# Performance work log

Measured on AMD Instinct MI355X. Metric: run time of the kernel, lower is better.

The kernel has to match this reference:

```python
import jax, jax.numpy as jnp
import numpy as np

N_NODES = 100000
N_EDGES = 1600000
D = 128          # in = hidden = out channels
N_LAYERS = 3


def setup_inputs() -> dict:
    key = jax.random.key(0)
    ks = jax.random.split(key, 20)
    inp = {
        "x": jax.random.normal(ks[0], (N_NODES, D), jnp.float32),
        "edge_index": jax.random.randint(ks[1], (2, N_EDGES), 0, N_NODES, dtype=jnp.int64),
    }
    s = 1.0 / np.sqrt(D)
    k = 2
    for l in range(N_LAYERS):
        inp[f"w1_{l}"] = jax.random.normal(ks[k], (D, D), jnp.float32) * s; k += 1
        inp[f"b1_{l}"] = jnp.zeros((D,), jnp.float32)
        inp[f"w2_{l}"] = jax.random.normal(ks[k], (D, D), jnp.float32) * s; k += 1
        inp[f"b2_{l}"] = jnp.zeros((D,), jnp.float32)
    # JK concat: 3 layers * D channels -> out D
    inp["jk_w"] = jax.random.normal(ks[k], (N_LAYERS * D, D), jnp.float32) * (1.0 / np.sqrt(N_LAYERS * D))
    inp["jk_b"] = jnp.zeros((D,), jnp.float32)
    return inp


def _gin_layer(x, src, dst, w1, b1, w2, b2):
    # GINConv, eps=0: h = (1+eps)*x + sum_{j in N(i)} x_j ; then MLP Lin-ReLU-Lin
    agg = jax.ops.segment_sum(x[src], dst, num_segments=N_NODES)  # [N, D]
    h = x + agg
    h = jax.nn.relu(h @ w1 + b1)
    return h @ w2 + b2


def reference(x, edge_index, w1_0, b1_0, w2_0, b2_0, w1_1, b1_1, w2_1, b2_1,
              w1_2, b1_2, w2_2, b2_2, jk_w, jk_b):
    src, dst = edge_index[0], edge_index[1]
    layers = [(w1_0, b1_0, w2_0, b2_0), (w1_1, b1_1, w2_1, b2_1), (w1_2, b1_2, w2_2, b2_2)]
    xs = []
    for i, (w1, b1, w2, b2) in enumerate(layers):
        # dropout is identity in eval mode
        residual = x  # skip_proj is Identity since in==out channels
        x = _gin_layer(x, src, dst, w1, b1, w2, b2) + residual
        if i != N_LAYERS - 1:
            x = jax.nn.elu(x)
        xs.append(x)
    x = jnp.concatenate(xs, axis=-1)  # JK 'cat' -> [N, 3*D]
    return x @ jk_w + jk_b
```

## Files before the change

### kernel.cpp

```cpp
#include <hip/hip_runtime.h>

typedef __bf16 bf16x8 __attribute__((ext_vector_type(8)));
typedef float f32x4 __attribute__((ext_vector_type(4)));

#define CHUNK 4096
#define NBUCK 512

struct WPack { const float* p[9]; };

__device__ inline __bf16 f2bf(float f){ return (__bf16)f; }

__global__ __launch_bounds__(256) void conv_w_kernel(WPack pk, __bf16* __restrict__ wf){
  int tid = blockIdx.x*256 + threadIdx.x;
  int m = tid >> 14;
  int r = tid & 16383;
  int j = r & 7;
  int lane = (r >> 3) & 63;
  int ks = (r >> 9) & 3;
  int c = r >> 11;
  int k = ks*32 + ((lane>>4)<<3) + j;
  int col = (c<<4) + (lane & 15);
  wf[tid] = f2bf(pk.p[m][k*128 + col]);
}

__global__ __launch_bounds__(256) void f2b_kernel(const float* __restrict__ x, __bf16* __restrict__ xb, int n8){
  int i = blockIdx.x*256 + threadIdx.x;
  if (i >= n8) return;
  f32x4 a = ((const f32x4*)x)[2*i];
  f32x4 b = ((const f32x4*)x)[2*i+1];
  bf16x8 r;
  r[0]=f2bf(a[0]); r[1]=f2bf(a[1]); r[2]=f2bf(a[2]); r[3]=f2bf(a[3]);
  r[4]=f2bf(b[0]); r[5]=f2bf(b[1]); r[6]=f2bf(b[2]); r[7]=f2bf(b[3]);
  ((bf16x8*)xb)[i] = r;
}

__global__ __launch_bounds__(256) void p1_count(const int* __restrict__ ei, int E, int NBLK,
    int* __restrict__ cnt){
  __shared__ int h[NBUCK];
  int b = blockIdx.x, t = threadIdx.x;
  h[t] = 0; h[t + 256] = 0;
  __syncthreads();
  int base = b*CHUNK;
  int lim = E - base; if (lim > CHUNK) lim = CHUNK;
  for (int i = t; i < lim; i += 256)
    atomicAdd(&h[ei[E + base + i] >> 8], 1);
  __syncthreads();
  cnt[t*NBLK + b] = h[t];
  cnt[(t + 256)*NBLK + b] = h[t + 256];
}

__global__ __launch_bounds__(256) void scan1_kernel(const int* __restrict__ cnt, int* __restrict__ bsum, int L){
  __shared__ int sh[256];
  int b = blockIdx.x, t = threadIdx.x;
  int base = b*2048 + t*8;
  int s = 0;
  #pragma unroll
  for (int j = 0; j < 8; j++){ int i = base + j; if (i < L) s += cnt[i]; }
  sh[t] = s; __syncthreads();
  for (int off = 128; off > 0; off >>= 1){
    if (t < off) sh[t] += sh[t + off];
    __syncthreads();
  }
  if (t == 0) bsum[b] = sh[0];
}

__global__ __launch_bounds__(256) void scan2_kernel(const int* __restrict__ bsum, int* __restrict__ boff,
                                                    int NB, int* __restrict__ total_out){
  __shared__ int sh[256];
  int t = threadIdx.x;
  int v = (t < NB) ? bsum[t] : 0;
  sh[t] = v; __syncthreads();
  for (int off = 1; off < 256; off <<= 1){
    int u = (t >= off) ? sh[t - off] : 0;
    __syncthreads();
    sh[t] += u;
    __syncthreads();
  }
  if (t < NB) boff[t] = sh[t] - v;
  if (t == 255) *total_out = sh[255];
}

__global__ __launch_bounds__(256) void scan3_kernel(const int* __restrict__ cnt, const int* __restrict__ boff,
                                                    int* __restrict__ off, int L){
  __shared__ int sh[256];
  int b = blockIdx.x, t = threadIdx.x;
  int base = b*2048 + t*8;
  int loc[8]; int s = 0;
  #pragma unroll
  for (int j = 0; j < 8; j++){ int i = base + j; int d = (i < L) ? cnt[i] : 0; loc[j] = d; s += d; }
  sh[t] = s; __syncthreads();
  for (int o = 1; o < 256; o <<= 1){
    int u = (t >= o) ? sh[t - o] : 0;
    __syncthreads();
    sh[t] += u;
    __syncthreads();
  }
  int excl = boff[b] + sh[t] - s;
  #pragma unroll
  for (int j = 0; j < 8; j++){ int i = base + j; if (i < L) off[i] = excl; excl += loc[j]; }
}

__global__ __launch_bounds__(256) void p3_scatter(const int* __restrict__ ei, int E, int NBLK,
    const int* __restrict__ off, int* __restrict__ tpack){
  __shared__ int cur[NBUCK];
  int b = blockIdx.x, t = threadIdx.x;
  cur[t]       = off[t*NBLK + b];
  cur[t + 256] = off[(t + 256)*NBLK + b];
  __syncthreads();
  int base = b*CHUNK;
  int lim = E - base; if (lim > CHUNK) lim = CHUNK;
  for (int i = t; i < lim; i += 256){
    int s = ei[base + i];
    int d = ei[E + base + i];
    int p = atomicAdd(&cur[d >> 8], 1);
    tpack[p] = (s << 8) | (d & 255);
  }
}

__global__ __launch_bounds__(256) void p4_build(const int* __restrict__ tpack,
    const int* __restrict__ off, int NBLK, int E, int N,
    int* __restrict__ rs, int* __restrict__ csr){
  __shared__ int dc[256], sc[256];
  int q = blockIdx.x, t = threadIdx.x;
  int bstart = off[q*NBLK];
  int bend = (q == NBUCK-1) ? E : off[(q+1)*NBLK];
  dc[t] = 0;
  __syncthreads();
  for (int i = bstart + t; i < bend; i += 256)
    atomicAdd(&dc[tpack[i] & 255], 1);
  __syncthreads();
  int v = dc[t];
  sc[t] = v; __syncthreads();
  for (int o = 1; o < 256; o <<= 1){
    int u = (t >= o) ? sc[t - o] : 0;
    __syncthreads();
    sc[t] += u;
    __syncthreads();
  }
  int ex = sc[t] - v;
  int gd = q*256 + t;
  if (gd < N) rs[gd] = bstart + ex;
  __syncthreads();
  dc[t] = ex;
  __syncthreads();
  for (int i = bstart + t; i < bend; i += 256){
    int p = tpack[i];
    int r = atomicAdd(&dc[p & 255], 1);
    csr[bstart + r] = p >> 8;
  }
}

__global__ __launch_bounds__(256) void agg_kernel(const __bf16* __restrict__ xb,
    const int* __restrict__ rs, const int* __restrict__ csr,
    __bf16* __restrict__ hb, int N)
{
  int node = blockIdx.x*4 + (threadIdx.x >> 6);
  if (node >= N) return;
  int lane = threadIdx.x & 63;
  int quad = lane >> 4;
  int l16  = lane & 15;
  int s = rs[node], e = rs[node+1];
  float a[8] = {0.f,0.f,0.f,0.f,0.f,0.f,0.f,0.f};
  for (int base = s; base < e; base += 64){
    int idx = base + lane;
    int nb = (idx < e) ? csr[idx] : 0;
    int cnt = e - base; if (cnt > 64) cnt = 64;
    int t = 0;
    for (; t + 8 <= cnt; t += 8){
      int sA = __shfl(nb, t + quad);
      int sB = __shfl(nb, t + 4 + quad);
      bf16x8 vA = ((const bf16x8*)(xb + (long)sA*128))[l16];
      bf16x8 vB = ((const bf16x8*)(xb + (long)sB*128))[l16];
      #pragma unroll
      for (int j = 0; j < 8; j++) a[j] += (float)vA[j] + (float)vB[j];
    }
    for (; t < cnt; t += 4){
      int i = t + quad;
      int ic = (i < cnt) ? i : (cnt - 1);
      int sA = __shfl(nb, ic);
      bf16x8 vA = ((const bf16x8*)(xb + (long)sA*128))[l16];
      if (i < cnt){
        #pragma unroll
        for (int j = 0; j < 8; j++) a[j] += (float)vA[j];
      }
    }
  }
  if (quad == 0){
    bf16x8 sv = ((const bf16x8*)(xb + (long)node*128))[l16];
    #pragma unroll
    for (int j = 0; j < 8; j++) a[j] += (float)sv[j];
  }
  #pragma unroll
  for (int j = 0; j < 8; j++){
    a[j] += __shfl_xor(a[j], 16);
    a[j] += __shfl_xor(a[j], 32);
  }
  if (quad == 0){
    bf16x8 r;
    #pragma unroll
    for (int j = 0; j < 8; j++) r[j] = f2bf(a[j]);
    ((bf16x8*)(hb + (long)node*128))[l16] = r;
  }
}

template<int ACT2>
__global__ __launch_bounds__(256) void fused_mlp(const __bf16* __restrict__ A,
    const __bf16* __restrict__ wf1, const __bf16* __restrict__ wf2,
    const float* __restrict__ b1, const float* __restrict__ b2,
    const __bf16* __restrict__ res, __bf16* __restrict__ out, int M)
{
  __shared__ __bf16 H[128][136];
  int lane = threadIdx.x & 63;
  int wid = threadIdx.x >> 6;
  long row0 = (long)blockIdx.x * 128;
  const bf16x8* w1v = (const bf16x8*)wf1;
  const bf16x8* w2v = (const bf16x8*)wf2;
  bf16x8 bv1[2][4], bv2[2][4];
  #pragma unroll
  for (int c2 = 0; c2 < 2; c2++)
    #pragma unroll
    for (int ks = 0; ks < 4; ks++){
      bv1[c2][ks] = w1v[((wid*2 + c2)*4 + ks)*64 + lane];
      bv2[c2][ks] = w2v[((wid*2 + c2)*4 + ks)*64 + lane];
    }
  int col0 = wid*32 + (lane & 15);
  float bb1_0 = b1[col0], bb1_1 = b1[col0 + 16];
  float bb2_0 = b2[col0], bb2_1 = b2[col0 + 16];
  int koff = (lane >> 4) << 3;
  #pragma unroll 2
  for (int rt = 0; rt < 8; rt++){
    long row = row0 + rt*16 + (lane & 15);
    long rowc = (row < M) ? row : (long)(M-1);
    const __bf16* ap = A + rowc*128 + koff;
    bf16x8 av[4];
    #pragma unroll
    for (int ks = 0; ks < 4; ks++)
      av[ks] = *(const bf16x8*)(ap + ks*32);
    f32x4 acc0 = {0.f,0.f,0.f,0.f}, acc1 = {0.f,0.f,0.f,0.f};
    #pragma unroll
    for (int ks = 0; ks < 4; ks++){
      acc0 = __builtin_amdgcn_mfma_f32_16x16x32_bf16(av[ks], bv1[0][ks], acc0, 0, 0, 0);
      acc1 = __builtin_amdgcn_mfma_f32_16x16x32_bf16(av[ks], bv1[1][ks], acc1, 0, 0, 0);
    }
    int r0 = rt*16 + ((lane >> 4) << 2);
    #pragma unroll
    for (int c2 = 0; c2 < 2; c2++){
      f32x4 acc = c2 ? acc1 : acc0;
      int col = col0 + c2*16;
      float bb = c2 ? bb1_1 : bb1_0;
      #pragma unroll
      for (int i = 0; i < 4; i++)
        H[r0 + i][col] = f2bf(fmaxf(acc[i] + bb, 0.f));
    }
  }
  __syncthreads();
  #pragma unroll 2
  for (int rt = 0; rt < 8; rt++){
    int r = rt*16 + (lane & 15);
    bf16x8 av[4];
    #pragma unroll
    for (int ks = 0; ks < 4; ks++)
      av[ks] = *(const bf16x8*)(&H[r][ks*32 + koff]);
    f32x4 acc0 = {0.f,0.f,0.f,0.f}, acc1 = {0.f,0.f,0.f,0.f};
    #pragma unroll
    for (int ks = 0; ks < 4; ks++){
      acc0 = __builtin_amdgcn_mfma_f32_16x16x32_bf16(av[ks], bv2[0][ks], acc0, 0, 0, 0);
      acc1 = __builtin_amdgcn_mfma_f32_16x16x32_bf16(av[ks], bv2[1][ks], acc1, 0, 0, 0);
    }
    long orow0 = row0 + rt*16 + ((lane >> 4) << 2);
    #pragma unroll
    for (int c2 = 0; c2 < 2; c2++){
      f32x4 acc = c2 ? acc1 : acc0;
      int col = col0 + c2*16;
      float bb = c2 ? bb2_1 : bb2_0;
      #pragma unroll
      for (int i = 0; i < 4; i++){
        long orow = orow0 + i;
        if (orow < M){
          long idx = orow*128 + col;
          float v = acc[i] + bb + (float)res[idx];
          if (ACT2 == 2) v = (v > 0.f) ? v : (__expf(v) - 1.f);
          out[idx] = f2bf(v);
        }
      }
    }
  }
}

__global__ __launch_bounds__(256) void jk_gemm(const __bf16* __restrict__ y1,
    const __bf16* __restrict__ y2, const __bf16* __restrict__ y3,
    const __bf16* __restrict__ wf, const float* __restrict__ bias,
    float* __restrict__ out, int M)
{
  int lane = threadIdx.x & 63;
  int wid = threadIdx.x >> 6;
  long row0 = (long)blockIdx.x * 128;
  const bf16x8* wfv = (const bf16x8*)wf;
  bf16x8 bv[2][12];
  #pragma unroll
  for (int c2 = 0; c2 < 2; c2++)
    #pragma unroll
    for (int ks = 0; ks < 12; ks++)
      bv[c2][ks] = wfv[(size_t)(6 + (ks>>2))*2048 + (size_t)((wid*2 + c2)*4 + (ks&3))*64 + lane];
  int col0 = wid*32 + (lane & 15);
  float b0 = bias[col0], b1 = bias[col0 + 16];
  int koff = (lane >> 4) << 3;
  const __bf16* ys[3] = {y1, y2, y3};
  #pragma unroll 1
  for (int rt = 0; rt < 8; rt++){
    long row = row0 + rt*16 + (lane & 15);
    long rowc = (row < M) ? row : (long)(M-1);
    f32x4 acc0 = {0.f,0.f,0.f,0.f}, acc1 = {0.f,0.f,0.f,0.f};
    #pragma unroll
    for (int ks = 0; ks < 12; ks++){
      bf16x8 av = *(const bf16x8*)(ys[ks>>2] + rowc*128 + (ks&3)*32 + koff);
      acc0 = __builtin_amdgcn_mfma_f32_16x16x32_bf16(av, bv[0][ks], acc0, 0, 0, 0);
      acc1 = __builtin_amdgcn_mfma_f32_16x16x32_bf16(av, bv[1][ks], acc1, 0, 0, 0);
    }
    long orow0 = row0 + rt*16 + ((lane >> 4) << 2);
    #pragma unroll
    for (int c2 = 0; c2 < 2; c2++){
      f32x4 acc = c2 ? acc1 : acc0;
      int col = col0 + c2*16;
      float bb = c2 ? b1 : b0;
      #pragma unroll
      for (int i = 0; i < 4; i++){
        long orow = orow0 + i;
        if (orow < M)
          out[orow*128 + col] = acc[i] + bb;
      }
    }
  }
}

extern "C" void kernel_launch(void* const* d_in, const int* in_sizes, int n_in,
                              void* d_out, int out_size, void* d_ws, size_t ws_size,
                              hipStream_t stream)
{
  const float* x   = (const float*)d_in[0];
  const int*   ei  = (const int*)d_in[1];
  const float* w1[3] = {(const float*)d_in[2], (const float*)d_in[6], (const float*)d_in[10]};
  const float* b1[3] = {(const float*)d_in[3], (const float*)d_in[7], (const float*)d_in[11]};
  const float* w2[3] = {(const float*)d_in[4], (const float*)d_in[8], (const float*)d_in[12]};
  const float* b2[3] = {(const float*)d_in[5], (const float*)d_in[9], (const float*)d_in[13]};
  const float* jkw = (const float*)d_in[14];
  const float* jkb = (const float*)d_in[15];
  int N = in_sizes[0] / 128;
  int E = in_sizes[1] / 2;
  float* outp = (float*)d_out;

  char* wptr = (char*)d_ws;
  auto alloc = [&](size_t bytes)->void*{
    void* p = (void*)wptr; wptr += (bytes + 255) & ~(size_t)255; return p;
  };
  int NBLK = (E + CHUNK - 1) / CHUNK;
  int L = NBUCK * NBLK;
  int* rs    = (int*)alloc((size_t)(N+1)*4);
  int* csr   = (int*)alloc((size_t)E*4);
  int* tpack = (int*)alloc((size_t)E*4);
  int* cnt   = (int*)alloc((size_t)L*4);
  int* off   = (int*)alloc((size_t)L*4);
  __bf16* y[4];
  for (int i = 0; i < 4; i++) y[i] = (__bf16*)alloc((size_t)N*128*2);
  __bf16* hb = (__bf16*)alloc((size_t)N*128*2);
  __bf16* wf = (__bf16*)alloc((size_t)9*16384*2);
  int nsb = (L + 2047) / 2048;
  int* bsum = (int*)alloc((size_t)nsb*4);
  int* boff = (int*)alloc((size_t)nsb*4);

  WPack pk;
  pk.p[0] = w1[0]; pk.p[1] = w2[0];
  pk.p[2] = w1[1]; pk.p[3] = w2[1];
  pk.p[4] = w1[2]; pk.p[5] = w2[2];
  pk.p[6] = jkw; pk.p[7] = jkw + 16384; pk.p[8] = jkw + 32768;
  conv_w_kernel<<<576, 256, 0, stream>>>(pk, wf);

  f2b_kernel<<<(N*128/8 + 255)/256, 256, 0, stream>>>(x, y[0], N*128/8);

  p1_count<<<NBLK, 256, 0, stream>>>(ei, E, NBLK, cnt);
  scan1_kernel<<<nsb, 256, 0, stream>>>(cnt, bsum, L);
  scan2_kernel<<<1, 256, 0, stream>>>(bsum, boff, nsb, rs + N);
  scan3_kernel<<<nsb, 256, 0, stream>>>(cnt, boff, off, L);
  p3_scatter<<<NBLK, 256, 0, stream>>>(ei, E, NBLK, off, tpack);
  p4_build<<<NBUCK, 256, 0, stream>>>(tpack, off, NBLK, E, N, rs, csr);

  int gemm_blocks = (N + 127)/128;
  for (int l = 0; l < 3; l++){
    agg_kernel<<<(N + 3)/4, 256, 0, stream>>>(y[l], rs, csr, hb, N);
    if (l < 2)
      fused_mlp<2><<<gemm_blocks, 256, 0, stream>>>(hb, wf + (size_t)(2*l)*16384, wf + (size_t)(2*l+1)*16384,
                                                    b1[l], b2[l], y[l], y[l+1], N);
    else
      fused_mlp<0><<<gemm_blocks, 256, 0, stream>>>(hb, wf + (size_t)(2*l)*16384, wf + (size_t)(2*l+1)*16384,
                                                    b1[l], b2[l], y[l], y[l+1], N);
  }
  jk_gemm<<<gemm_blocks, 256, 0, stream>>>(y[1], y[2], y[3], wf, jkb, outp, N);
}
```

Before: 428.6 us.

## Fuse last GIN layer MLP with JK projection and merge prep kernels

The final layer's MLP now feeds the JK concat GEMM directly. Its output stays in shared memory, so the y3 buffer is never written to or re-read from global memory, and one launch is removed. The weight-conversion and input-conversion kernels are merged into a single launch, and the aggregation inner loop gets an unroll-2 pragma. In exchange the fused kernel uses about 68KB of LDS per block and holds more weight registers, which may lower occupancy.

```diff
diff --git a/kernel.cpp b/kernel.cpp
--- a/kernel.cpp
+++ b/kernel.cpp
@@ -10,28 +10,30 @@
 
 __device__ inline __bf16 f2bf(float f){ return (__bf16)f; }
 
-__global__ __launch_bounds__(256) void conv_w_kernel(WPack pk, __bf16* __restrict__ wf){
-  int tid = blockIdx.x*256 + threadIdx.x;
-  int m = tid >> 14;
-  int r = tid & 16383;
-  int j = r & 7;
-  int lane = (r >> 3) & 63;
-  int ks = (r >> 9) & 3;
-  int c = r >> 11;
-  int k = ks*32 + ((lane>>4)<<3) + j;
-  int col = (c<<4) + (lane & 15);
-  wf[tid] = f2bf(pk.p[m][k*128 + col]);
-}
-
-__global__ __launch_bounds__(256) void f2b_kernel(const float* __restrict__ x, __bf16* __restrict__ xb, int n8){
-  int i = blockIdx.x*256 + threadIdx.x;
-  if (i >= n8) return;
-  f32x4 a = ((const f32x4*)x)[2*i];
-  f32x4 b = ((const f32x4*)x)[2*i+1];
-  bf16x8 r;
-  r[0]=f2bf(a[0]); r[1]=f2bf(a[1]); r[2]=f2bf(a[2]); r[3]=f2bf(a[3]);
-  r[4]=f2bf(b[0]); r[5]=f2bf(b[1]); r[6]=f2bf(b[2]); r[7]=f2bf(b[3]);
-  ((bf16x8*)xb)[i] = r;
+__global__ __launch_bounds__(256) void prep_kernel(WPack pk, __bf16* __restrict__ wf,
+    const float* __restrict__ x, __bf16* __restrict__ xb, int n8){
+  int b = blockIdx.x, t = threadIdx.x;
+  if (b < 576){
+    int tid = b*256 + t;
+    int m = tid >> 14;
+    int r = tid & 16383;
+    int j = r & 7;
+    int lane = (r >> 3) & 63;
+    int ks = (r >> 9) & 3;
+    int c = r >> 11;
+    int k = ks*32 + ((lane>>4)<<3) + j;
+    int col = (c<<4) + (lane & 15);
+    wf[tid] = f2bf(pk.p[m][k*128 + col]);
+  } else {
+    int i = (b - 576)*256 + t;
+    if (i >= n8) return;
+    f32x4 a = ((const f32x4*)x)[2*i];
+    f32x4 bb = ((const f32x4*)x)[2*i+1];
+    bf16x8 r;
+    r[0]=f2bf(a[0]); r[1]=f2bf(a[1]); r[2]=f2bf(a[2]); r[3]=f2bf(a[3]);
+    r[4]=f2bf(bb[0]); r[5]=f2bf(bb[1]); r[6]=f2bf(bb[2]); r[7]=f2bf(bb[3]);
+    ((bf16x8*)xb)[i] = r;
+  }
 }
 
 __global__ __launch_bounds__(256) void p1_count(const int* __restrict__ ei, int E, int NBLK,
@@ -166,6 +168,7 @@
     int nb = (idx < e) ? csr[idx] : 0;
     int cnt = e - base; if (cnt > 64) cnt = 64;
     int t = 0;
+    #pragma unroll 2
     for (; t + 8 <= cnt; t += 8){
       int sA = __shfl(nb, t + quad);
       int sB = __shfl(nb, t + 4 + quad);
@@ -287,42 +290,117 @@
   }
 }
 
-__global__ __launch_bounds__(256) void jk_gemm(const __bf16* __restrict__ y1,
-    const __bf16* __restrict__ y2, const __bf16* __restrict__ y3,
-    const __bf16* __restrict__ wf, const float* __restrict__ bias,
-    float* __restrict__ out, int M)
+__global__ __launch_bounds__(256) void fused_mlp_jk(const __bf16* __restrict__ A,
+    const __bf16* __restrict__ y1g, const __bf16* __restrict__ y2g,
+    const __bf16* __restrict__ wf1, const __bf16* __restrict__ wf2,
+    const __bf16* __restrict__ wfjk,
+    const float* __restrict__ b1, const float* __restrict__ b2,
+    const float* __restrict__ jkb, float* __restrict__ out, int M)
 {
+  __shared__ __bf16 H[128][136];
+  __shared__ __bf16 Y3[128][136];
   int lane = threadIdx.x & 63;
   int wid = threadIdx.x >> 6;
   long row0 = (long)blockIdx.x * 128;
-  const bf16x8* wfv = (const bf16x8*)wf;
-  bf16x8 bv[2][12];
+  const bf16x8* w1v = (const bf16x8*)wf1;
+  const bf16x8* w2v = (const bf16x8*)wf2;
+  bf16x8 bv1[2][4], bv2[2][4];
   #pragma unroll
   for (int c2 = 0; c2 < 2; c2++)
     #pragma unroll
+    for (int ks = 0; ks < 4; ks++){
+      bv1[c2][ks] = w1v[((wid*2 + c2)*4 + ks)*64 + lane];
+      bv2[c2][ks] = w2v[((wid*2 + c2)*4 + ks)*64 + lane];
+    }
+  int col0 = wid*32 + (lane & 15);
+  float bb1_0 = b1[col0], bb1_1 = b1[col0 + 16];
+  float bb2_0 = b2[col0], bb2_1 = b2[col0 + 16];
+  int koff = (lane >> 4) << 3;
+  #pragma unroll 2
+  for (int rt = 0; rt < 8; rt++){
+    long row = row0 + rt*16 + (lane & 15);
+    long rowc = (row < M) ? row : (long)(M-1);
+    const __bf16* ap = A + rowc*128 + koff;
+    bf16x8 av[4];
+    #pragma unroll
+    for (int ks = 0; ks < 4; ks++)
+      av[ks] = *(const bf16x8*)(ap + ks*32);
+    f32x4 acc0 = {0.f,0.f,0.f,0.f}, acc1 = {0.f,0.f,0.f,0.f};
+    #pragma unroll
+    for (int ks = 0; ks < 4; ks++){
+      acc0 = __builtin_amdgcn_mfma_f32_16x16x32_bf16(av[ks], bv1[0][ks], acc0, 0, 0, 0);
+      acc1 = __builtin_amdgcn_mfma_f32_16x16x32_bf16(av[ks], bv1[1][ks], acc1, 0, 0, 0);
+    }
+    int r0 = rt*16 + ((lane >> 4) << 2);
+    #pragma unroll
+    for (int c2 = 0; c2 < 2; c2++){
+      f32x4 acc = c2 ? acc1 : acc0;
+      int col = col0 + c2*16;
+      float bb = c2 ? bb1_1 : bb1_0;
+      #pragma unroll
+      for (int i = 0; i < 4; i++)
+        H[r0 + i][col] = f2bf(fmaxf(acc[i] + bb, 0.f));
+    }
+  }
+  __syncthreads();
+  #pragma unroll 2
+  for (int rt = 0; rt < 8; rt++){
+    int r = rt*16 + (lane & 15);
+    bf16x8 av[4];
+    #pragma unroll
+    for (int ks = 0; ks < 4; ks++)
+      av[ks] = *(const bf16x8*)(&H[r][ks*32 + koff]);
+    f32x4 acc0 = {0.f,0.f,0.f,0.f}, acc1 = {0.f,0.f,0.f,0.f};
+    #pragma unroll
+    for (int ks = 0; ks < 4; ks++){
+      acc0 = __builtin_amdgcn_mfma_f32_16x16x32_bf16(av[ks], bv2[0][ks], acc0, 0, 0, 0);
+      acc1 = __builtin_amdgcn_mfma_f32_16x16x32_bf16(av[ks], bv2[1][ks], acc1, 0, 0, 0);
+    }
+    long orow0 = row0 + rt*16 + ((lane >> 4) << 2);
+    int r0 = rt*16 + ((lane >> 4) << 2);
+    #pragma unroll
+    for (int c2 = 0; c2 < 2; c2++){
+      f32x4 acc = c2 ? acc1 : acc0;
+      int col = col0 + c2*16;
+      float bb = c2 ? bb2_1 : bb2_0;
+      #pragma unroll
+      for (int i = 0; i < 4; i++){
+        long orow = orow0 + i;
+        float rv = (orow < M) ? (float)y2g[orow*128 + col] : 0.f;
+        Y3[r0 + i][col] = f2bf(acc[i] + bb + rv);
+      }
+    }
+  }
+  __syncthreads();
+  const bf16x8* wjv = (const bf16x8*)wfjk;
+  bf16x8 bvj[2][12];
+  #pragma unroll
+  for (int c2 = 0; c2 < 2; c2++)
+    #pragma unroll
     for (int ks = 0; ks < 12; ks++)
-      bv[c2][ks] = wfv[(size_t)(6 + (ks>>2))*2048 + (size_t)((wid*2 + c2)*4 + (ks&3))*64 + lane];
-  int col0 = wid*32 + (lane & 15);
-  float b0 = bias[col0], b1 = bias[col0 + 16];
-  int koff = (lane >> 4) << 3;
-  const __bf16* ys[3] = {y1, y2, y3};
+      bvj[c2][ks] = wjv[(size_t)(ks>>2)*2048 + (size_t)((wid*2 + c2)*4 + (ks&3))*64 + lane];
+  float jb0 = jkb[col0], jb1 = jkb[col0 + 16];
   #pragma unroll 1
   for (int rt = 0; rt < 8; rt++){
     long row = row0 + rt*16 + (lane & 15);
     long rowc = (row < M) ? row : (long)(M-1);
+    int rl = rt*16 + (lane & 15);
     f32x4 acc0 = {0.f,0.f,0.f,0.f}, acc1 = {0.f,0.f,0.f,0.f};
     #pragma unroll
     for (int ks = 0; ks < 12; ks++){
-      bf16x8 av = *(const bf16x8*)(ys[ks>>2] + rowc*128 + (ks&3)*32 + koff);
-      acc0 = __builtin_amdgcn_mfma_f32_16x16x32_bf16(av, bv[0][ks], acc0, 0, 0, 0);
-      acc1 = __builtin_amdgcn_mfma_f32_16x16x32_bf16(av, bv[1][ks], acc1, 0, 0, 0);
+      bf16x8 av;
+      if (ks < 4)      av = *(const bf16x8*)(y1g + rowc*128 + ks*32 + koff);
+      else if (ks < 8) av = *(const bf16x8*)(y2g + rowc*128 + (ks-4)*32 + koff);
+      else             av = *(const bf16x8*)(&Y3[rl][(ks-8)*32 + koff]);
+      acc0 = __builtin_amdgcn_mfma_f32_16x16x32_bf16(av, bvj[0][ks], acc0, 0, 0, 0);
+      acc1 = __builtin_amdgcn_mfma_f32_16x16x32_bf16(av, bvj[1][ks], acc1, 0, 0, 0);
     }
     long orow0 = row0 + rt*16 + ((lane >> 4) << 2);
     #pragma unroll
     for (int c2 = 0; c2 < 2; c2++){
       f32x4 acc = c2 ? acc1 : acc0;
       int col = col0 + c2*16;
-      float bb = c2 ? b1 : b0;
+      float bb = c2 ? jb1 : jb0;
       #pragma unroll
       for (int i = 0; i < 4; i++){
         long orow = orow0 + i;
@@ -360,8 +438,8 @@
   int* tpack = (int*)alloc((size_t)E*4);
   int* cnt   = (int*)alloc((size_t)L*4);
   int* off   = (int*)alloc((size_t)L*4);
-  __bf16* y[4];
-  for (int i = 0; i < 4; i++) y[i] = (__bf16*)alloc((size_t)N*128*2);
+  __bf16* y[3];
+  for (int i = 0; i < 3; i++) y[i] = (__bf16*)alloc((size_t)N*128*2);
   __bf16* hb = (__bf16*)alloc((size_t)N*128*2);
   __bf16* wf = (__bf16*)alloc((size_t)9*16384*2);
   int nsb = (L + 2047) / 2048;
@@ -373,9 +451,8 @@
   pk.p[2] = w1[1]; pk.p[3] = w2[1];
   pk.p[4] = w1[2]; pk.p[5] = w2[2];
   pk.p[6] = jkw; pk.p[7] = jkw + 16384; pk.p[8] = jkw + 32768;
-  conv_w_kernel<<<576, 256, 0, stream>>>(pk, wf);
-
-  f2b_kernel<<<(N*128/8 + 255)/256, 256, 0, stream>>>(x, y[0], N*128/8);
+  int n8 = N*128/8;
+  prep_kernel<<<576 + (n8 + 255)/256, 256, 0, stream>>>(pk, wf, x, y[0], n8);
 
   p1_count<<<NBLK, 256, 0, stream>>>(ei, E, NBLK, cnt);
   scan1_kernel<<<nsb, 256, 0, stream>>>(cnt, bsum, L);
@@ -391,8 +468,8 @@
       fused_mlp<2><<<gemm_blocks, 256, 0, stream>>>(hb, wf + (size_t)(2*l)*16384, wf + (size_t)(2*l+1)*16384,
                                                     b1[l], b2[l], y[l], y[l+1], N);
     else
-      fused_mlp<0><<<gemm_blocks, 256, 0, stream>>>(hb, wf + (size_t)(2*l)*16384, wf + (size_t)(2*l+1)*16384,
-                                                    b1[l], b2[l], y[l], y[l+1], N);
-  }
-  jk_gemm<<<gemm_blocks, 256, 0, stream>>>(y[1], y[2], y[3], wf, jkb, outp, N);
-}
+      fused_mlp_jk<<<gemm_blocks, 256, 0, stream>>>(hb, y[1], y[2],
+                                                    wf + (size_t)4*16384, wf + (size_t)5*16384, wf + (size_t)6*16384,
+                                                    b1[2], b2[2], jkb, outp, N);
+  }
+}
```

Result: faster. 404.0 us (-5.7%).
